# Kernel tuning notes

Measured on AMD Instinct MI355X. Metric: run time of the kernel, lower is better.

Reference implementation:

```python
import jax, jax.numpy as jnp
import numpy as np

T, B, Y, H, R, L = 256, 1024, 32, 1024, 512, 2  # seq_len, batch, y_dim, h_dim, rnn_dim, n_layers


def setup_inputs() -> dict:
    key = jax.random.key(0)
    ks = jax.random.split(key, 18)
    s = jnp.float32(0.05)

    def w(k, shape):
        return jax.random.normal(k, shape, dtype=jnp.float32) * s

    return {
        "y": jax.random.normal(ks[0], (T, B, Y), dtype=jnp.float32),
        # decoder MLP: Linear(R->H), ReLU, Linear(H->H), ReLU
        "dec_w1": w(ks[1], (H, R)), "dec_b1": jnp.zeros((H,), jnp.float32),
        "dec_w2": w(ks[2], (H, H)), "dec_b2": jnp.zeros((H,), jnp.float32),
        # dec_mean: Linear(H->Y); dec_std: Linear(H->Y) + Softplus
        "mean_w": w(ks[3], (Y, H)), "mean_b": jnp.zeros((Y,), jnp.float32),
        "std_w": w(ks[4], (Y, H)), "std_b": jnp.zeros((Y,), jnp.float32),
        # 2-layer GRU, torch gate order (r, z, n)
        "gru_wih0": w(ks[5], (3 * R, Y)), "gru_whh0": w(ks[6], (3 * R, R)),
        "gru_bih0": jnp.zeros((3 * R,), jnp.float32), "gru_bhh0": jnp.zeros((3 * R,), jnp.float32),
        "gru_wih1": w(ks[7], (3 * R, R)), "gru_whh1": w(ks[8], (3 * R, R)),
        "gru_bih1": jnp.zeros((3 * R,), jnp.float32), "gru_bhh1": jnp.zeros((3 * R,), jnp.float32),
    }


def _gru_cell(x, h, wih, whh, bih, bhh):
    # torch GRUCell math, gates ordered (r, z, n)
    gi = x @ wih.T + bih          # [B, 3R]
    gh = h @ whh.T + bhh          # [B, 3R]
    ir, iz, inn = jnp.split(gi, 3, axis=-1)
    hr, hz, hn = jnp.split(gh, 3, axis=-1)
    r = jax.nn.sigmoid(ir + hr)
    z = jax.nn.sigmoid(iz + hz)
    n = jnp.tanh(inn + r * hn)
    return (1.0 - z) * n + z * h


def reference(y, dec_w1, dec_b1, dec_w2, dec_b2, mean_w, mean_b, std_w, std_b,
              gru_wih0, gru_whh0, gru_bih0, gru_bhh0,
              gru_wih1, gru_whh1, gru_bih1, gru_bhh1):
    log2pi = jnp.float32(np.log(2.0 * np.pi))
    batch = y.shape[1]
    h0 = jnp.zeros((L, batch, R), dtype=y.dtype)

    def step(carry, y_t):
        h, nll = carry
        # decode from top-layer hidden state (before the GRU update)
        d = jax.nn.relu(h[-1] @ dec_w1.T + dec_b1)
        d = jax.nn.relu(d @ dec_w2.T + dec_b2)
        mean_t = d @ mean_w.T + mean_b
        std_t = jax.nn.softplus(d @ std_w.T + std_b)
        # nll_gauss: 0.5 * sum((x-mu)^2/std^2 + 2*log(std) + log(2*pi))
        nll_t = 0.5 * jnp.sum((y_t - mean_t) ** 2 / (std_t ** 2)
                              + 2.0 * jnp.log(std_t) + log2pi)
        # single GRU step (2 layers)
        h_l0 = _gru_cell(y_t, h[0], gru_wih0, gru_whh0, gru_bih0, gru_bhh0)
        h_l1 = _gru_cell(h_l0, h[1], gru_wih1, gru_whh1, gru_bih1, gru_bhh1)
        return (jnp.stack([h_l0, h_l1]), nll + nll_t), None

    (_, nll), _ = jax.lax.scan(step, (h0, jnp.float32(0.0)), y)
    return nll
```

## Files before the change

### kernel.cpp

```cpp
#include <hip/hip_runtime.h>
#include <math.h>

#define TT   256
#define BB   1024
#define YDIM 32
#define HDIM 1024
#define RDIM 512

typedef __attribute__((ext_vector_type(8))) short frag8;
typedef __attribute__((ext_vector_type(4))) float f32x4;

#define LDS_BUF 16384

#define OFF_NLL   ((size_t)0)
#define OFF_HAF   ((size_t)4096)
#define SZ_HF     ((size_t)BB*RDIM*4)
#define OFF_HBF   (OFF_HAF + 2*SZ_HF)
#define OFF_HA16  (OFF_HBF + 2*SZ_HF)
#define SZ_H16    ((size_t)BB*RDIM*2)
#define OFF_HB16  (OFF_HA16 + 2*SZ_H16)
#define OFF_D1    (OFF_HB16 + 2*SZ_H16)
#define SZ_DBUF   ((size_t)BB*HDIM*2)
#define OFF_D2    (OFF_D1 + 2*SZ_DBUF)
#define OFF_Y16   (OFF_D2 + 2*SZ_DBUF)
#define OFF_WG0I  (OFF_Y16 + (size_t)TT*BB*YDIM*2)
#define OFF_WG0H  (OFF_WG0I + (size_t)1536*YDIM*2)
#define OFF_WG1I  (OFF_WG0H + (size_t)1536*RDIM*2)
#define OFF_WG1H  (OFF_WG1I + (size_t)1536*RDIM*2)
#define OFF_WD1   (OFF_WG1H + (size_t)1536*RDIM*2)
#define OFF_WD2   (OFF_WD1 + (size_t)HDIM*RDIM*2)
#define OFF_WMS   (OFF_WD2 + (size_t)HDIM*HDIM*2)
#define OFF_BI0   (OFF_WMS + (size_t)64*HDIM*2)
#define OFF_BH0   (OFF_BI0 + 1536*4)
#define OFF_BI1   (OFF_BH0 + 1536*4)
#define OFF_BH1   (OFF_BI1 + 1536*4)

__device__ __forceinline__ short f2bf(float f) {
  union { float f; unsigned u; } v; v.f = f;
  unsigned r = (v.u + 0x7fffu + ((v.u >> 16) & 1u)) >> 16;
  return (short)r;
}
__device__ __forceinline__ void cvt8(const float* s, short* d) {
  float4 a = *(const float4*)s;
  float4 b = *(const float4*)(s + 4);
  frag8 v;
  v[0]=f2bf(a.x); v[1]=f2bf(a.y); v[2]=f2bf(a.z); v[3]=f2bf(a.w);
  v[4]=f2bf(b.x); v[5]=f2bf(b.y); v[6]=f2bf(b.z); v[7]=f2bf(b.w);
  *(frag8*)d = v;
}
__device__ __forceinline__ int permRow(int n) {
  int q = n / 48, r = n - 48 * q, g = r >> 4, u = r & 15;
  return g * 512 + q * 16 + u;
}
__device__ __forceinline__ float sigf(float x) { return 1.0f / (1.0f + expf(-x)); }

__device__ __forceinline__ void gload16(const short* g, short* l) {
  __builtin_amdgcn_global_load_lds(
      (const __attribute__((address_space(1))) void*)g,
      (__attribute__((address_space(3))) void*)l, 16, 0, 0);
}

template<int MF, int NF>
__device__ __forceinline__ void kloop64(
    const short* __restrict__ A, int lda, int m0,
    const short* __restrict__ B, int ldb, int nrowsB, int K,
    int wm, int wn, short* lds, f32x4 (*acc)[NF], int tid)
{
  const int l = tid & 63, w = tid >> 6, u = l & 15, quad = l >> 4;
  const int nk = K >> 6;
  const int bunits = nrowsB << 3;

  auto stage = [&](int kc, int buf) {
    short* base = lds + buf * LDS_BUF;
    const int k0 = kc << 6;
    for (int c = (w << 6); c < 1024; c += 256) {
      int p = c + l, r = p >> 3, q = (p & 7) ^ (r & 7);
      gload16(A + (size_t)(m0 + r) * lda + k0 + (q << 3), base + (c << 3));
    }
    short* bb = base + 8192;
    for (int c = (w << 6); c < bunits; c += 256) {
      int p = c + l, r = p >> 3, q = (p & 7) ^ (r & 7);
      gload16(B + (size_t)r * ldb + k0 + (q << 3), bb + (c << 3));
    }
  };

  stage(0, 0);
  __syncthreads();
  for (int kc = 0; kc < nk; ++kc) {
    if (kc + 1 < nk) stage(kc + 1, (kc + 1) & 1);
    const short* base = lds + (kc & 1) * LDS_BUF;
#pragma unroll
    for (int kk2 = 0; kk2 < 2; ++kk2) {
      const int q = (kk2 << 2) + quad;
      const int aoff = (q ^ (u & 7)) << 3;
      frag8 a[MF], b[NF];
#pragma unroll
      for (int i = 0; i < MF; ++i)
        a[i] = *(const frag8*)(base + ((wm + (i << 4) + u) << 6) + aoff);
#pragma unroll
      for (int f = 0; f < NF; ++f)
        b[f] = *(const frag8*)(base + 8192 + ((wn + (f << 4) + u) << 6) + aoff);
#pragma unroll
      for (int i = 0; i < MF; ++i)
#pragma unroll
        for (int f = 0; f < NF; ++f)
          acc[i][f] = __builtin_amdgcn_mfma_f32_16x16x32_bf16(a[i], b[f], acc[i][f], 0, 0, 0);
    }
    __syncthreads();
  }
}

template<int MF, int NF>
__device__ __forceinline__ void kloop32(
    const short* __restrict__ A, int lda, int m0,
    const short* __restrict__ B, int nrowsB,
    int wm, int wn, short* lds, f32x4 (*acc)[NF], int tid)
{
  const int l = tid & 63, w = tid >> 6, u = l & 15, quad = l >> 4;
  short* base = lds;
  for (int c = (w << 6); c < 512; c += 256) {
    int p = c + l, r = p >> 2, q = (p & 3) ^ (r & 3);
    gload16(A + (size_t)(m0 + r) * lda + (q << 3), base + (c << 3));
  }
  short* bb = base + 4096;
  const int bunits = nrowsB << 2;
  for (int c = (w << 6); c < bunits; c += 256) {
    int p = c + l, r = p >> 2, q = (p & 3) ^ (r & 3);
    gload16(B + (size_t)r * 32 + (q << 3), bb + (c << 3));
  }
  __syncthreads();
  const int aoff = (quad ^ (u & 3)) << 3;
  frag8 a[MF], b[NF];
#pragma unroll
  for (int i = 0; i < MF; ++i)
    a[i] = *(const frag8*)(base + ((wm + (i << 4) + u) << 5) + aoff);
#pragma unroll
  for (int f = 0; f < NF; ++f)
    b[f] = *(const frag8*)(base + 4096 + ((wn + (f << 4) + u) << 5) + aoff);
#pragma unroll
  for (int i = 0; i < MF; ++i)
#pragma unroll
    for (int f = 0; f < NF; ++f)
      acc[i][f] = __builtin_amdgcn_mfma_f32_16x16x32_bf16(a[i], b[f], acc[i][f], 0, 0, 0);
  __syncthreads();
}

template<bool GI32>
__device__ void gru_tile(int mb, int nb,
                         const short* Ax, int ldx, const short* Wgi,
                         const short* Ah, const short* Wgh,
                         const float* bi, const float* bh,
                         const float* hold, float* hout, short* h16out,
                         short* lds, int tid)
{
  f32x4 zero = {0.f, 0.f, 0.f, 0.f};
  f32x4 gi[4][3], gh[4][3];
#pragma unroll
  for (int i = 0; i < 4; ++i)
#pragma unroll
    for (int f = 0; f < 3; ++f) { gi[i][f] = zero; gh[i][f] = zero; }
  const int w = tid >> 6, l = tid & 63, u = l & 15, quad = l >> 4;
  const int wm = (w & 1) * 64, wn = (w >> 1) * 48;
  if (GI32)
    kloop32<4, 3>(Ax, ldx, mb * 128, Wgi, 96, wm, wn, lds, gi, tid);
  else
    kloop64<4, 3>(Ax, ldx, mb * 128, Wgi, RDIM, 96, RDIM, wm, wn, lds, gi, tid);
  kloop64<4, 3>(Ah, RDIM, mb * 128, Wgh, RDIM, 96, RDIM, wm, wn, lds, gh, tid);

  const int np = nb * 96 + (w >> 1) * 48 + u;
  const float bir = bi[np], biz = bi[np + 16], bin = bi[np + 32];
  const float bhr = bh[np], bhz = bh[np + 16], bhn = bh[np + 32];
  const int unit = nb * 32 + (w >> 1) * 16 + u;
#pragma unroll
  for (int i = 0; i < 4; ++i)
#pragma unroll
    for (int j = 0; j < 4; ++j) {
      int row = mb * 128 + wm + 16 * i + quad * 4 + j;
      float r = sigf((gi[i][0][j] + bir) + (gh[i][0][j] + bhr));
      float z = sigf((gi[i][1][j] + biz) + (gh[i][1][j] + bhz));
      float n = tanhf((gi[i][2][j] + bin) + r * (gh[i][2][j] + bhn));
      float ho = hold[(size_t)row * RDIM + unit];
      float hn = (1.f - z) * n + z * ho;
      hout[(size_t)row * RDIM + unit] = hn;
      h16out[(size_t)row * RDIM + unit] = f2bf(hn);
    }
}

__device__ void dec_tile(int mb, int nb, const short* A, int lda, int K,
                         const short* W, const float* bias, short* outp,
                         short* lds, int tid)
{
  f32x4 zero = {0.f, 0.f, 0.f, 0.f};
  f32x4 acc[4][4];
#pragma unroll
  for (int i = 0; i < 4; ++i)
#pragma unroll
    for (int f = 0; f < 4; ++f) acc[i][f] = zero;
  const int w = tid >> 6, l = tid & 63, u = l & 15, quad = l >> 4;
  const int wm = (w & 1) * 64, wn = (w >> 1) * 64;
  kloop64<4, 4>(A, lda, mb * 128, W, K, 128, K, wm, wn, lds, acc, tid);
  const int colb = nb * 128 + wn + u;
  float bv[4];
#pragma unroll
  for (int f = 0; f < 4; ++f) bv[f] = bias[colb + 16 * f];
#pragma unroll
  for (int i = 0; i < 4; ++i)
#pragma unroll
    for (int f = 0; f < 4; ++f)
#pragma unroll
      for (int j = 0; j < 4; ++j) {
        int row = mb * 128 + wm + 16 * i + quad * 4 + j;
        float v = acc[i][f][j] + bv[f];
        if (v < 0.f) v = 0.f;
        outp[(size_t)row * HDIM + colb + 16 * f] = f2bf(v);
      }
}

__device__ void ms_tile(int mb, int tstep, const short* d2p, const short* Wms,
                        const float* mbias, const float* sbias, const float* y,
                        float* nll, short* lds, int tid)
{
  f32x4 zero = {0.f, 0.f, 0.f, 0.f};
  f32x4 acc[2][4];
#pragma unroll
  for (int i = 0; i < 2; ++i)
#pragma unroll
    for (int f = 0; f < 4; ++f) acc[i][f] = zero;
  const int w = tid >> 6, l = tid & 63, u = l & 15, quad = l >> 4;
  kloop64<2, 4>(d2p, HDIM, mb * 128, Wms, HDIM, 64, HDIM, w * 32, 0, lds, acc, tid);
  float lsum = 0.f;
#pragma unroll
  for (int i = 0; i < 2; ++i)
#pragma unroll
    for (int j = 0; j < 4; ++j) {
      int row = mb * 128 + w * 32 + 16 * i + quad * 4 + j;
      const float* yr = y + ((size_t)tstep * BB + row) * YDIM;
#pragma unroll
      for (int f = 0; f < 2; ++f) {
        int c = 16 * f + u;
        float m  = acc[i][f][j] + mbias[c];
        float sp = acc[i][f + 2][j] + sbias[c];
        float sg = (sp > 20.f) ? sp : log1pf(expf(sp));
        float dv = (yr[c] - m) / sg;
        lsum += dv * dv + 2.f * logf(sg) + 1.8378770664093453f;
      }
    }
  lsum *= 0.5f;
#pragma unroll
  for (int o = 32; o; o >>= 1) lsum += __shfl_xor(lsum, o);
  if (l == 0) atomicAdd(nll, lsum);
}

__global__ __launch_bounds__(256) void prepack_kernel(
    const float* y, const float* dw1, const float* dw2,
    const float* mw, const float* sw,
    const float* wih0, const float* whh0, const float* bih0, const float* bhh0,
    const float* wih1, const float* whh1, const float* bih1, const float* bhh1,
    char* __restrict__ ws)
{
  const size_t g = (size_t)blockIdx.x * 256 + threadIdx.x;
  const size_t N = (size_t)gridDim.x * 256;
  float4 z4 = {0.f, 0.f, 0.f, 0.f};
  float4* hz = (float4*)(ws + OFF_HAF);
  for (size_t i = g; i < (size_t)4 * BB * RDIM / 4; i += N) hz[i] = z4;
  int4 zi = {0, 0, 0, 0};
  int4* h16z = (int4*)(ws + OFF_HA16);
  for (size_t i = g; i < (size_t)4 * BB * RDIM / 8; i += N) h16z[i] = zi;
  if (g == 0) *(float*)(ws + OFF_NLL) = 0.f;

  short* y16  = (short*)(ws + OFF_Y16);
  short* Wg0i = (short*)(ws + OFF_WG0I);
  short* Wg0h = (short*)(ws + OFF_WG0H);
  short* Wg1i = (short*)(ws + OFF_WG1I);
  short* Wg1h = (short*)(ws + OFF_WG1H);
  short* Wd1  = (short*)(ws + OFF_WD1);
  short* Wd2  = (short*)(ws + OFF_WD2);
  short* Wms  = (short*)(ws + OFF_WMS);
  float* bi0  = (float*)(ws + OFF_BI0);
  float* bh0  = (float*)(ws + OFF_BH0);
  float* bi1  = (float*)(ws + OFF_BI1);
  float* bh1  = (float*)(ws + OFF_BH1);

  for (size_t s = g; s < (size_t)TT * BB * YDIM / 8; s += N)
    cvt8(y + s * 8, y16 + s * 8);
  for (size_t s = g; s < (size_t)1536 * RDIM / 8; s += N) {
    int row = (int)(s >> 6), seg = (int)(s & 63) << 3;
    int pr = permRow(row);
    cvt8(whh0 + (size_t)pr * RDIM + seg, Wg0h + (size_t)row * RDIM + seg);
    cvt8(wih1 + (size_t)pr * RDIM + seg, Wg1i + (size_t)row * RDIM + seg);
    cvt8(whh1 + (size_t)pr * RDIM + seg, Wg1h + (size_t)row * RDIM + seg);
  }
  for (size_t s = g; s < (size_t)1536 * YDIM / 8; s += N) {
    int row = (int)(s >> 2), seg = (int)(s & 3) << 3;
    cvt8(wih0 + (size_t)permRow(row) * YDIM + seg, Wg0i + (size_t)row * YDIM + seg);
  }
  for (size_t s = g; s < (size_t)HDIM * RDIM / 8; s += N)
    cvt8(dw1 + s * 8, Wd1 + s * 8);
  for (size_t s = g; s < (size_t)HDIM * HDIM / 8; s += N)
    cvt8(dw2 + s * 8, Wd2 + s * 8);
  for (size_t s = g; s < (size_t)64 * HDIM / 8; s += N) {
    int row = (int)(s >> 7), seg = (int)(s & 127) << 3;
    const float* src = (row < 32) ? (mw + (size_t)row * HDIM + seg)
                                  : (sw + (size_t)(row - 32) * HDIM + seg);
    cvt8(src, Wms + (size_t)row * HDIM + seg);
  }
  for (size_t s = g; s < 1536; s += N) {
    int pr = permRow((int)s);
    bi0[s] = bih0[pr]; bh0[s] = bhh0[pr];
    bi1[s] = bih1[pr]; bh1[s] = bhh1[pr];
  }
}

__global__ __launch_bounds__(256, 2) void phase_kernel(
    int p, const float* __restrict__ y,
    const float* db1, const float* db2, const float* mbias, const float* sbias,
    char* __restrict__ ws)
{
  __shared__ short lds[2 * LDS_BUF];
  const int tid = threadIdx.x;
  const int t = blockIdx.x;
  const int cur = p & 1, prv = cur ^ 1;

  float* hAf = (float*)(ws + OFF_HAF);
  float* hBf = (float*)(ws + OFF_HBF);
  short* hA16 = (short*)(ws + OFF_HA16);
  short* hB16 = (short*)(ws + OFF_HB16);
  short* d10 = (short*)(ws + OFF_D1);
  short* d20 = (short*)(ws + OFF_D2);
  const short* y16 = (const short*)(ws + OFF_Y16);

  float* hAfc = hAf + (size_t)cur * BB * RDIM;
  float* hAfp = hAf + (size_t)prv * BB * RDIM;
  float* hBfc = hBf + (size_t)cur * BB * RDIM;
  float* hBfp = hBf + (size_t)prv * BB * RDIM;
  short* hA16c = hA16 + (size_t)cur * BB * RDIM;
  short* hA16p = hA16 + (size_t)prv * BB * RDIM;
  short* hB16c = hB16 + (size_t)cur * BB * RDIM;
  short* hB16p = hB16 + (size_t)prv * BB * RDIM;
  short* d1c = d10 + (size_t)cur * BB * HDIM;
  short* d1p = d10 + (size_t)prv * BB * HDIM;
  short* d2c = d20 + (size_t)cur * BB * HDIM;
  short* d2p = d20 + (size_t)prv * BB * HDIM;

  const short* Wg0i = (const short*)(ws + OFF_WG0I);
  const short* Wg0h = (const short*)(ws + OFF_WG0H);
  const short* Wg1i = (const short*)(ws + OFF_WG1I);
  const short* Wg1h = (const short*)(ws + OFF_WG1H);
  const short* Wd1  = (const short*)(ws + OFF_WD1);
  const short* Wd2  = (const short*)(ws + OFF_WD2);
  const short* Wms  = (const short*)(ws + OFF_WMS);
  const float* bi0  = (const float*)(ws + OFF_BI0);
  const float* bh0  = (const float*)(ws + OFF_BH0);
  const float* bi1  = (const float*)(ws + OFF_BI1);
  const float* bh1  = (const float*)(ws + OFF_BH1);
  float* nllp = (float*)(ws + OFF_NLL);

  if (t < 128) {
    if (p >= 1 && p <= 255) {
      int mb = t >> 4, nb = t & 15;
      gru_tile<false>(mb, nb,
                      hA16p, RDIM, Wg1i + (size_t)nb * 96 * RDIM,
                      hB16p, Wg1h + (size_t)nb * 96 * RDIM,
                      bi1, bh1, hBfp, hBfc, hB16c, lds, tid);
    }
  } else if (t < 192) {
    if (p >= 2 && p <= 257) {
      int q = t - 128, mb = q >> 3, nb = q & 7;
      dec_tile(mb, nb, d1p, HDIM, HDIM, Wd2 + (size_t)nb * 128 * HDIM,
               db2, d2c, lds, tid);
    }
  } else if (t < 200) {
    if (p >= 3 && p <= 258) {
      ms_tile(t - 192, p - 3, d2p, Wms, mbias, sbias, y, nllp, lds, tid);
    }
  } else if (t < 328) {
    if (p <= 255) {
      int q = t - 200, mb = q >> 4, nb = q & 15;
      gru_tile<true>(mb, nb,
                     y16 + (size_t)p * BB * YDIM, YDIM, Wg0i + (size_t)nb * 96 * YDIM,
                     hA16p, Wg0h + (size_t)nb * 96 * RDIM,
                     bi0, bh0, hAfp, hAfc, hA16c, lds, tid);
    }
  } else {
    if (p >= 1 && p <= 256) {
      int q = t - 328, mb = q >> 3, nb = q & 7;
      dec_tile(mb, nb, hB16p, RDIM, RDIM, Wd1 + (size_t)nb * 128 * RDIM,
               db1, d1c, lds, tid);
    }
  }
}

__global__ void finish_kernel(float* out, const char* ws)
{
  if (threadIdx.x == 0 && blockIdx.x == 0)
    out[0] = *(const float*)(ws + OFF_NLL);
}

extern "C" void kernel_launch(void* const* d_in, const int* in_sizes, int n_in,
                              void* d_out, int out_size, void* d_ws, size_t ws_size,
                              hipStream_t stream) {
  (void)in_sizes; (void)n_in; (void)out_size; (void)ws_size;
  const float* y    = (const float*)d_in[0];
  const float* dw1  = (const float*)d_in[1];
  const float* db1  = (const float*)d_in[2];
  const float* dw2  = (const float*)d_in[3];
  const float* db2  = (const float*)d_in[4];
  const float* mw   = (const float*)d_in[5];
  const float* mbias= (const float*)d_in[6];
  const float* sw   = (const float*)d_in[7];
  const float* sbias= (const float*)d_in[8];
  const float* wih0 = (const float*)d_in[9];
  const float* whh0 = (const float*)d_in[10];
  const float* bih0 = (const float*)d_in[11];
  const float* bhh0 = (const float*)d_in[12];
  const float* wih1 = (const float*)d_in[13];
  const float* whh1 = (const float*)d_in[14];
  const float* bih1 = (const float*)d_in[15];
  const float* bhh1 = (const float*)d_in[16];
  char* ws = (char*)d_ws;
  float* out = (float*)d_out;

  prepack_kernel<<<256, 256, 0, stream>>>(y, dw1, dw2, mw, sw,
                                          wih0, whh0, bih0, bhh0,
                                          wih1, whh1, bih1, bhh1, ws);
  for (int p = 0; p < 259; ++p)
    phase_kernel<<<392, 256, 0, stream>>>(p, y, db1, db2, mbias, sbias, ws);
  finish_kernel<<<1, 1, 0, stream>>>(out, ws);
}
```

Before: 5.794 ms.

## Replace per-phase launches with a persistent cooperative kernel using grid sync

```diff
diff --git a/kernel.cpp b/kernel.cpp
--- a/kernel.cpp
+++ b/kernel.cpp
@@ -1,5 +1,8 @@
 #include <hip/hip_runtime.h>
+#include <hip/hip_cooperative_groups.h>
 #include <math.h>
+
+namespace cg = cooperative_groups;
 
 #define TT   256
 #define BB   1024
@@ -145,13 +148,13 @@
   __syncthreads();
 }
 
-template<bool GI32>
+template<bool GI32, bool RS>
 __device__ void gru_tile(int mb, int nb,
                          const short* Ax, int ldx, const short* Wgi,
                          const short* Ah, const short* Wgh,
                          const float* bi, const float* bh,
-                         const float* hold, float* hout, short* h16out,
-                         short* lds, int tid)
+                         const float* hold, float* hout, float* hreg,
+                         short* h16out, short* lds, int tid)
 {
   f32x4 zero = {0.f, 0.f, 0.f, 0.f};
   f32x4 gi[4][3], gh[4][3];
@@ -179,9 +182,10 @@
       float r = sigf((gi[i][0][j] + bir) + (gh[i][0][j] + bhr));
       float z = sigf((gi[i][1][j] + biz) + (gh[i][1][j] + bhz));
       float n = tanhf((gi[i][2][j] + bin) + r * (gh[i][2][j] + bhn));
-      float ho = hold[(size_t)row * RDIM + unit];
+      float ho = RS ? hreg[i * 4 + j] : hold[(size_t)row * RDIM + unit];
       float hn = (1.f - z) * n + z * ho;
-      hout[(size_t)row * RDIM + unit] = hn;
+      if (RS) hreg[i * 4 + j] = hn;
+      else    hout[(size_t)row * RDIM + unit] = hn;
       h16out[(size_t)row * RDIM + unit] = f2bf(hn);
     }
 }
@@ -311,6 +315,95 @@
   }
 }
 
+__global__ __launch_bounds__(256, 2) void mega_kernel(
+    const float* __restrict__ y,
+    const float* db1, const float* db2, const float* mbias, const float* sbias,
+    char* __restrict__ ws)
+{
+  __shared__ short lds[2 * LDS_BUF];
+  const int tid = threadIdx.x;
+  const int xcd = blockIdx.x & 7;
+  const int slot = blockIdx.x >> 3;
+
+  int role = -1, mb = 0, nb = 0;
+  if (xcd < 3) {
+    const int cnt = (xcd == 0) ? 6 : 5;
+    if (slot < cnt * 8) { role = 0; nb = 3 * (slot >> 3) + xcd; mb = slot & 7; }
+  } else if (xcd == 3) { role = 1; nb = 2 * (slot >> 3);     mb = slot & 7; }
+  else if (xcd == 4)   { role = 1; nb = 2 * (slot >> 3) + 1; mb = slot & 7; }
+  else if (xcd == 5) {
+    if (slot < 32)      { role = 2; nb = slot >> 3; mb = slot & 7; }
+    else if (slot < 40) { role = 4; mb = slot - 32; }
+  } else if (xcd == 6) {
+    if (slot < 32)      { role = 2; nb = 4 + (slot >> 3); mb = slot & 7; }
+    else if (slot < 40) { role = 3; nb = 0; mb = slot - 32; }
+  } else {
+    if (slot < 56)      { role = 3; nb = 1 + (slot >> 3); mb = slot & 7; }
+  }
+
+  short* hA16 = (short*)(ws + OFF_HA16);
+  short* hB16 = (short*)(ws + OFF_HB16);
+  short* d10 = (short*)(ws + OFF_D1);
+  short* d20 = (short*)(ws + OFF_D2);
+  const short* y16 = (const short*)(ws + OFF_Y16);
+  const short* Wg0i = (const short*)(ws + OFF_WG0I);
+  const short* Wg0h = (const short*)(ws + OFF_WG0H);
+  const short* Wg1i = (const short*)(ws + OFF_WG1I);
+  const short* Wg1h = (const short*)(ws + OFF_WG1H);
+  const short* Wd1  = (const short*)(ws + OFF_WD1);
+  const short* Wd2  = (const short*)(ws + OFF_WD2);
+  const short* Wms  = (const short*)(ws + OFF_WMS);
+  const float* bi0  = (const float*)(ws + OFF_BI0);
+  const float* bh0  = (const float*)(ws + OFF_BH0);
+  const float* bi1  = (const float*)(ws + OFF_BI1);
+  const float* bh1  = (const float*)(ws + OFF_BH1);
+  float* nllp = (float*)(ws + OFF_NLL);
+
+  float hreg[16];
+#pragma unroll
+  for (int i = 0; i < 16; ++i) hreg[i] = 0.f;
+
+  cg::grid_group grid = cg::this_grid();
+
+  for (int p = 0; p < 259; ++p) {
+    const int cur = p & 1, prv = cur ^ 1;
+    short* hA16c = hA16 + (size_t)cur * BB * RDIM;
+    short* hA16p = hA16 + (size_t)prv * BB * RDIM;
+    short* hB16c = hB16 + (size_t)cur * BB * RDIM;
+    short* hB16p = hB16 + (size_t)prv * BB * RDIM;
+    short* d1c = d10 + (size_t)cur * BB * HDIM;
+    short* d1p = d10 + (size_t)prv * BB * HDIM;
+    short* d2c = d20 + (size_t)cur * BB * HDIM;
+    short* d2p = d20 + (size_t)prv * BB * HDIM;
+
+    if (role == 0) {
+      if (p >= 1 && p <= 255)
+        gru_tile<false, true>(mb, nb,
+                              hA16p, RDIM, Wg1i + (size_t)nb * 96 * RDIM,
+                              hB16p, Wg1h + (size_t)nb * 96 * RDIM,
+                              bi1, bh1, nullptr, nullptr, hreg, hB16c, lds, tid);
+    } else if (role == 1) {
+      if (p <= 255)
+        gru_tile<true, true>(mb, nb,
+                             y16 + (size_t)p * BB * YDIM, YDIM, Wg0i + (size_t)nb * 96 * YDIM,
+                             hA16p, Wg0h + (size_t)nb * 96 * RDIM,
+                             bi0, bh0, nullptr, nullptr, hreg, hA16c, lds, tid);
+    } else if (role == 2) {
+      if (p >= 2 && p <= 257)
+        dec_tile(mb, nb, d1p, HDIM, HDIM, Wd2 + (size_t)nb * 128 * HDIM,
+                 db2, d2c, lds, tid);
+    } else if (role == 3) {
+      if (p >= 1 && p <= 256)
+        dec_tile(mb, nb, hB16p, RDIM, RDIM, Wd1 + (size_t)nb * 128 * RDIM,
+                 db1, d1c, lds, tid);
+    } else if (role == 4) {
+      if (p >= 3 && p <= 258)
+        ms_tile(mb, p - 3, d2p, Wms, mbias, sbias, y, nllp, lds, tid);
+    }
+    grid.sync();
+  }
+}
+
 __global__ __launch_bounds__(256, 2) void phase_kernel(
     int p, const float* __restrict__ y,
     const float* db1, const float* db2, const float* mbias, const float* sbias,
@@ -358,10 +451,10 @@
   if (t < 128) {
     if (p >= 1 && p <= 255) {
       int mb = t >> 4, nb = t & 15;
-      gru_tile<false>(mb, nb,
-                      hA16p, RDIM, Wg1i + (size_t)nb * 96 * RDIM,
-                      hB16p, Wg1h + (size_t)nb * 96 * RDIM,
-                      bi1, bh1, hBfp, hBfc, hB16c, lds, tid);
+      gru_tile<false, false>(mb, nb,
+                             hA16p, RDIM, Wg1i + (size_t)nb * 96 * RDIM,
+                             hB16p, Wg1h + (size_t)nb * 96 * RDIM,
+                             bi1, bh1, hBfp, hBfc, nullptr, hB16c, lds, tid);
     }
   } else if (t < 192) {
     if (p >= 2 && p <= 257) {
@@ -376,10 +469,10 @@
   } else if (t < 328) {
     if (p <= 255) {
       int q = t - 200, mb = q >> 4, nb = q & 15;
-      gru_tile<true>(mb, nb,
-                     y16 + (size_t)p * BB * YDIM, YDIM, Wg0i + (size_t)nb * 96 * YDIM,
-                     hA16p, Wg0h + (size_t)nb * 96 * RDIM,
-                     bi0, bh0, hAfp, hAfc, hA16c, lds, tid);
+      gru_tile<true, false>(mb, nb,
+                            y16 + (size_t)p * BB * YDIM, YDIM, Wg0i + (size_t)nb * 96 * YDIM,
+                            hA16p, Wg0h + (size_t)nb * 96 * RDIM,
+                            bi0, bh0, hAfp, hAfc, nullptr, hA16c, lds, tid);
     }
   } else {
     if (p >= 1 && p <= 256) {
@@ -423,7 +516,16 @@
   prepack_kernel<<<256, 256, 0, stream>>>(y, dw1, dw2, mw, sw,
                                           wih0, whh0, bih0, bhh0,
                                           wih1, whh1, bih1, bhh1, ws);
-  for (int p = 0; p < 259; ++p)
-    phase_kernel<<<392, 256, 0, stream>>>(p, y, db1, db2, mbias, sbias, ws);
+
+  void* kargs[] = { (void*)&y, (void*)&db1, (void*)&db2,
+                    (void*)&mbias, (void*)&sbias, (void*)&ws };
+  hipError_t e = hipLaunchCooperativeKernel((void*)mega_kernel,
+                                            dim3(512), dim3(256),
+                                            kargs, 0, stream);
+  if (e != hipSuccess) {
+    (void)hipGetLastError();
+    for (int p = 0; p < 259; ++p)
+      phase_kernel<<<392, 256, 0, stream>>>(p, y, db1, db2, mbias, sbias, ws);
+  }
   finish_kernel<<<1, 1, 0, stream>>>(out, ws);
 }
```

Result: slower. 19.87 ms (+242.9%).

## Decouple GRU recurrence from decoder and batch decoder GEMMs over time chunks

Applied to the files above, without the earlier changes.

```diff
diff --git a/kernel.cpp b/kernel.cpp
--- a/kernel.cpp
+++ b/kernel.cpp
@@ -6,6 +6,7 @@
 #define YDIM 32
 #define HDIM 1024
 #define RDIM 512
+#define CH   32
 
 typedef __attribute__((ext_vector_type(8))) short frag8;
 typedef __attribute__((ext_vector_type(4))) float f32x4;
@@ -34,6 +35,12 @@
 #define OFF_BH0   (OFF_BI0 + 1536*4)
 #define OFF_BI1   (OFF_BH0 + 1536*4)
 #define OFF_BH1   (OFF_BI1 + 1536*4)
+#define OFF_H1ALL (OFF_BH1 + 4096)
+#define SZ_H1ALL  ((size_t)TT*BB*RDIM*2)
+#define OFF_D1CH  (OFF_H1ALL + SZ_H1ALL)
+#define SZ_CHB    ((size_t)CH*BB*HDIM*2)
+#define OFF_D2CH  (OFF_D1CH + SZ_CHB)
+#define OFF_END   (OFF_D2CH + SZ_CHB)
 
 __device__ __forceinline__ short f2bf(float f) {
   union { float f; unsigned u; } v; v.f = f;
@@ -216,8 +223,8 @@
       }
 }
 
-__device__ void ms_tile(int mb, int tstep, const short* d2p, const short* Wms,
-                        const float* mbias, const float* sbias, const float* y,
+__device__ void ms_tile(int mb, const short* d2p, const short* Wms,
+                        const float* mbias, const float* sbias, const float* ybase,
                         float* nll, short* lds, int tid)
 {
   f32x4 zero = {0.f, 0.f, 0.f, 0.f};
@@ -234,7 +241,7 @@
 #pragma unroll
     for (int j = 0; j < 4; ++j) {
       int row = mb * 128 + w * 32 + 16 * i + quad * 4 + j;
-      const float* yr = y + ((size_t)tstep * BB + row) * YDIM;
+      const float* yr = ybase + (size_t)row * YDIM;
 #pragma unroll
       for (int f = 0; f < 2; ++f) {
         int c = 16 * f + u;
@@ -256,7 +263,7 @@
     const float* mw, const float* sw,
     const float* wih0, const float* whh0, const float* bih0, const float* bhh0,
     const float* wih1, const float* whh1, const float* bih1, const float* bhh1,
-    char* __restrict__ ws)
+    char* __restrict__ ws, int big)
 {
   const size_t g = (size_t)blockIdx.x * 256 + threadIdx.x;
   const size_t N = (size_t)gridDim.x * 256;
@@ -266,6 +273,10 @@
   int4 zi = {0, 0, 0, 0};
   int4* h16z = (int4*)(ws + OFF_HA16);
   for (size_t i = g; i < (size_t)4 * BB * RDIM / 8; i += N) h16z[i] = zi;
+  if (big) {
+    int4* h1z = (int4*)(ws + OFF_H1ALL);
+    for (size_t i = g; i < (size_t)BB * RDIM / 8; i += N) h1z[i] = zi;
+  }
   if (g == 0) *(float*)(ws + OFF_NLL) = 0.f;
 
   short* y16  = (short*)(ws + OFF_Y16);
@@ -311,6 +322,88 @@
   }
 }
 
+__global__ __launch_bounds__(256, 2) void recur_kernel(int p, char* __restrict__ ws)
+{
+  __shared__ short lds[2 * LDS_BUF];
+  const int tid = threadIdx.x;
+  const int xcd = blockIdx.x & 7;
+  const int slot = blockIdx.x >> 3;
+  const int cur = p & 1, prv = cur ^ 1;
+
+  float* hAf = (float*)(ws + OFF_HAF);
+  float* hBf = (float*)(ws + OFF_HBF);
+  short* hA16 = (short*)(ws + OFF_HA16);
+  short* h1all = (short*)(ws + OFF_H1ALL);
+  const short* y16 = (const short*)(ws + OFF_Y16);
+  const short* Wg0i = (const short*)(ws + OFF_WG0I);
+  const short* Wg0h = (const short*)(ws + OFF_WG0H);
+  const short* Wg1i = (const short*)(ws + OFF_WG1I);
+  const short* Wg1h = (const short*)(ws + OFF_WG1H);
+  const float* bi0  = (const float*)(ws + OFF_BI0);
+  const float* bh0  = (const float*)(ws + OFF_BH0);
+  const float* bi1  = (const float*)(ws + OFF_BI1);
+  const float* bh1  = (const float*)(ws + OFF_BH1);
+
+  const int nb = (xcd & 3) * 4 + (slot & 3);
+  const int mb = slot >> 2;
+
+  if (xcd < 4) {
+    if (p >= 1) {
+      gru_tile<false>(mb, nb,
+                      hA16 + (size_t)prv * BB * RDIM, RDIM, Wg1i + (size_t)nb * 96 * RDIM,
+                      h1all + (size_t)(p - 1) * BB * RDIM, Wg1h + (size_t)nb * 96 * RDIM,
+                      bi1, bh1,
+                      hBf + (size_t)prv * BB * RDIM, hBf + (size_t)cur * BB * RDIM,
+                      h1all + (size_t)p * BB * RDIM, lds, tid);
+    }
+  } else {
+    if (p <= 254) {
+      gru_tile<true>(mb, nb,
+                     y16 + (size_t)p * BB * YDIM, YDIM, Wg0i + (size_t)nb * 96 * YDIM,
+                     hA16 + (size_t)prv * BB * RDIM, Wg0h + (size_t)nb * 96 * RDIM,
+                     bi0, bh0,
+                     hAf + (size_t)prv * BB * RDIM, hAf + (size_t)cur * BB * RDIM,
+                     hA16 + (size_t)cur * BB * RDIM, lds, tid);
+    }
+  }
+}
+
+__global__ __launch_bounds__(256, 2) void d1_kernel(int c_, const float* db1, char* __restrict__ ws)
+{
+  __shared__ short lds[2 * LDS_BUF];
+  const int tid = threadIdx.x;
+  const int xcd = blockIdx.x & 7, slot = blockIdx.x >> 3;
+  const int mt = xcd * 32 + (slot >> 3), nb = slot & 7;
+  const short* A = (const short*)(ws + OFF_H1ALL) + (size_t)c_ * CH * BB * RDIM;
+  const short* Wd1 = (const short*)(ws + OFF_WD1);
+  short* d1ch = (short*)(ws + OFF_D1CH);
+  dec_tile(mt, nb, A, RDIM, RDIM, Wd1 + (size_t)nb * 128 * RDIM, db1, d1ch, lds, tid);
+}
+
+__global__ __launch_bounds__(256, 2) void d2_kernel(int c_, const float* db2, char* __restrict__ ws)
+{
+  __shared__ short lds[2 * LDS_BUF];
+  const int tid = threadIdx.x;
+  const int xcd = blockIdx.x & 7, slot = blockIdx.x >> 3;
+  const int mt = xcd * 32 + (slot >> 3), nb = slot & 7;
+  const short* d1ch = (const short*)(ws + OFF_D1CH);
+  const short* Wd2 = (const short*)(ws + OFF_WD2);
+  short* d2ch = (short*)(ws + OFF_D2CH);
+  dec_tile(mt, nb, d1ch, HDIM, HDIM, Wd2 + (size_t)nb * 128 * HDIM, db2, d2ch, lds, tid);
+}
+
+__global__ __launch_bounds__(256, 2) void msd_kernel(int c_, const float* mbias, const float* sbias,
+                                                     const float* y, char* __restrict__ ws)
+{
+  __shared__ short lds[2 * LDS_BUF];
+  const int tid = threadIdx.x;
+  const int mb = (blockIdx.x & 7) * 32 + (blockIdx.x >> 3);
+  const short* d2ch = (const short*)(ws + OFF_D2CH);
+  const short* Wms = (const short*)(ws + OFF_WMS);
+  float* nllp = (float*)(ws + OFF_NLL);
+  ms_tile(mb, d2ch, Wms, mbias, sbias, y + (size_t)c_ * CH * BB * YDIM, nllp, lds, tid);
+}
+
 __global__ __launch_bounds__(256, 2) void phase_kernel(
     int p, const float* __restrict__ y,
     const float* db1, const float* db2, const float* mbias, const float* sbias,
@@ -371,7 +464,8 @@
     }
   } else if (t < 200) {
     if (p >= 3 && p <= 258) {
-      ms_tile(t - 192, p - 3, d2p, Wms, mbias, sbias, y, nllp, lds, tid);
+      ms_tile(t - 192, d2p, Wms, mbias, sbias,
+              y + (size_t)(p - 3) * BB * YDIM, nllp, lds, tid);
     }
   } else if (t < 328) {
     if (p <= 255) {
@@ -399,7 +493,7 @@
 extern "C" void kernel_launch(void* const* d_in, const int* in_sizes, int n_in,
                               void* d_out, int out_size, void* d_ws, size_t ws_size,
                               hipStream_t stream) {
-  (void)in_sizes; (void)n_in; (void)out_size; (void)ws_size;
+  (void)in_sizes; (void)n_in; (void)out_size;
   const float* y    = (const float*)d_in[0];
   const float* dw1  = (const float*)d_in[1];
   const float* db1  = (const float*)d_in[2];
@@ -420,10 +514,22 @@
   char* ws = (char*)d_ws;
   float* out = (float*)d_out;
 
+  const int big = (ws_size >= OFF_END) ? 1 : 0;
+
   prepack_kernel<<<256, 256, 0, stream>>>(y, dw1, dw2, mw, sw,
                                           wih0, whh0, bih0, bhh0,
-                                          wih1, whh1, bih1, bhh1, ws);
-  for (int p = 0; p < 259; ++p)
-    phase_kernel<<<392, 256, 0, stream>>>(p, y, db1, db2, mbias, sbias, ws);
+                                          wih1, whh1, bih1, bhh1, ws, big);
+  if (big) {
+    for (int p = 0; p < 256; ++p)
+      recur_kernel<<<256, 256, 0, stream>>>(p, ws);
+    for (int c_ = 0; c_ < TT / CH; ++c_) {
+      d1_kernel<<<2048, 256, 0, stream>>>(c_, db1, ws);
+      d2_kernel<<<2048, 256, 0, stream>>>(c_, db2, ws);
+      msd_kernel<<<256, 256, 0, stream>>>(c_, mbias, sbias, y, ws);
+    }
+  } else {
+    for (int p = 0; p < 259; ++p)
+      phase_kernel<<<392, 256, 0, stream>>>(p, y, db1, db2, mbias, sbias, ws);
+  }
   finish_kernel<<<1, 1, 0, stream>>>(out, ws);
 }
```

Result: slower. 6.921 ms (+19.5%).
